# Optimization experiments

Hardware: AMD Instinct MI355X
Metric: run time of the kernel (lower is better)

## Reference

```python
import jax, jax.numpy as jnp
import numpy as np

B = 16          # batch
N = 48          # protein_length
K = 7           # window_size (odd)
PAD = (K - 1) // 2
L = 4 * N - 3   # lattice side from SparseTensor dense_shape
LP = L + 2 * PAD  # zero-padded lattice so every KxKxK window is in-bounds


def setup_inputs() -> dict:
    key = jax.random.key(0)
    k1, k2, k3 = jax.random.split(key, 3)
    acids = jax.random.uniform(k1, (B, N), dtype=jnp.float32)
    mask = jax.random.randint(k2, (B, N), 0, 2).astype(bool)
    # raw integer lattice coords; module maps them via 2*(idx + N-1) into [0, 4N-4]
    idx = jax.random.randint(k3, (B, N, 3), 0, N)
    return {"acids": acids, "mask": mask, "idx": idx}


def _extract_snake(acids, mask, idx2, inter_values, inter_mask, inter_idx):
    # Per-sample: scatter masked acid values + interpolated midpoint values
    # into a dense zero-padded lattice, then gather a KxKxK window around
    # each residue coordinate.  Matches sparse scatter + sparse_slice/to_dense.
    lat = jnp.zeros((LP, LP, LP), dtype=acids.dtype)
    # masked-out rows -> out-of-range index LP, dropped by mode='drop'
    a_idx = jnp.where(mask[:, None], idx2 + PAD, LP)          # [N,3]
    lat = lat.at[a_idx[:, 0], a_idx[:, 1], a_idx[:, 2]].set(acids, mode='drop')
    i_idx = jnp.where(inter_mask[:, None], inter_idx + PAD, LP)  # [N-1,3]
    lat = lat.at[i_idx[:, 0], i_idx[:, 1], i_idx[:, 2]].set(inter_values, mode='drop')

    def window(c):  # c: [3] int, window offset idx2-PAD in unpadded coords == idx2 in padded
        return jax.lax.dynamic_slice(lat, (c[0], c[1], c[2]), (K, K, K))

    regions = jax.vmap(window)(idx2)                          # [N,K,K,K]
    return regions * mask[:, None, None, None].astype(acids.dtype)


def reference(acids, mask, idx):
    idx2 = 2 * (idx + (N - 1))                                # even coords in [0, 4N-4]
    # AVG pool window 2 VALID over sequence dim; midpoints of even coords are exact ints
    inter_idx = (idx2[:, :-1] + idx2[:, 1:]) // 2             # [B,N-1,3]
    # 2 * avg(adjacent acids) + 1 == sum + 1
    inter_values = acids[:, :-1] + acids[:, 1:] + 1.0         # [B,N-1]
    inter_mask = mask[:, 1:]                                  # [B,N-1]
    out = jax.vmap(_extract_snake)(acids, mask, idx2, inter_values, inter_mask, inter_idx)
    return out[..., None]                                     # [B,N,K,K,K,1]
```

## Files before the change

kernel.cpp:

```cpp
#include <hip/hip_runtime.h>

#define BB 16
#define NN 48
#define KK 7
#define PADP 3
#define KCUBE (KK * KK * KK)

__global__ __launch_bounds__(384) void LatticeSnake_kernel(
    const float* __restrict__ acids,
    const int* __restrict__ mask,
    const int* __restrict__ idx,
    float* __restrict__ out)
{
    const int blk = blockIdx.x;
    const int b = blk / NN;
    const int i = blk % NN;
    const int t = threadIdx.x;

    __shared__ int s_idx2[NN][3];
    __shared__ float s_ac[NN];
    __shared__ int s_mk[NN];
    __shared__ int s_ii[NN - 1][3];
    __shared__ float s_iv[NN - 1];

    if (t < NN) {
        s_ac[t] = acids[b * NN + t];
        s_mk[t] = mask[b * NN + t];
#pragma unroll
        for (int d = 0; d < 3; ++d)
            s_idx2[t][d] = 2 * (idx[(b * NN + t) * 3 + d] + (NN - 1));
    }
    __syncthreads();
    if (t < NN - 1) {
#pragma unroll
        for (int d = 0; d < 3; ++d)
            s_ii[t][d] = (s_idx2[t][d] + s_idx2[t + 1][d]) >> 1;
        s_iv[t] = s_ac[t] + s_ac[t + 1] + 1.0f;
    }
    __syncthreads();

    if (t < KCUBE) {
        const int oz = t % KK;
        const int oy = (t / KK) % KK;
        const int ox = t / (KK * KK);
        const int qx = s_idx2[i][0] + ox - PADP;
        const int qy = s_idx2[i][1] + oy - PADP;
        const int qz = s_idx2[i][2] + oz - PADP;

        float v = 0.0f;
        for (int j = 0; j < NN; ++j) {
            if (s_mk[j] && s_idx2[j][0] == qx && s_idx2[j][1] == qy &&
                s_idx2[j][2] == qz)
                v = s_ac[j];
        }
        for (int j = 0; j < NN - 1; ++j) {
            if (s_mk[j + 1] && s_ii[j][0] == qx && s_ii[j][1] == qy &&
                s_ii[j][2] == qz)
                v = s_iv[j];
        }
        if (!s_mk[i]) v = 0.0f;
        out[blk * KCUBE + t] = v;
    }
}

extern "C" void kernel_launch(void* const* d_in, const int* in_sizes, int n_in,
                              void* d_out, int out_size, void* d_ws, size_t ws_size,
                              hipStream_t stream) {
    const float* acids = (const float*)d_in[0];
    const int* mask = (const int*)d_in[1];
    const int* idx = (const int*)d_in[2];
    float* out = (float*)d_out;

    dim3 grid(BB * NN);
    dim3 block(384);
    LatticeSnake_kernel<<<grid, block, 0, stream>>>(acids, mask, idx, out);
}
```

Baseline: 64.50 us.

## Replace per-cell linear search with shared-memory scatter into window

```diff
diff --git a/kernel.cpp b/kernel.cpp
--- a/kernel.cpp
+++ b/kernel.cpp
@@ -22,6 +22,7 @@
     __shared__ int s_mk[NN];
     __shared__ int s_ii[NN - 1][3];
     __shared__ float s_iv[NN - 1];
+    __shared__ int s_win[KCUBE];
 
     if (t < NN) {
         s_ac[t] = acids[b * NN + t];
@@ -30,7 +31,9 @@
         for (int d = 0; d < 3; ++d)
             s_idx2[t][d] = 2 * (idx[(b * NN + t) * 3 + d] + (NN - 1));
     }
+    if (t < KCUBE) s_win[t] = 0;
     __syncthreads();
+
     if (t < NN - 1) {
 #pragma unroll
         for (int d = 0; d < 3; ++d)
@@ -39,26 +42,34 @@
     }
     __syncthreads();
 
+    const int bx = s_idx2[i][0], by = s_idx2[i][1], bz = s_idx2[i][2];
+    if (t < NN) {
+        if (s_mk[t]) {
+            const int ox = s_idx2[t][0] - bx + PADP;
+            const int oy = s_idx2[t][1] - by + PADP;
+            const int oz = s_idx2[t][2] - bz + PADP;
+            if (((unsigned)ox < KK) & ((unsigned)oy < KK) & ((unsigned)oz < KK))
+                atomicMax(&s_win[(ox * KK + oy) * KK + oz], t + 1);
+        }
+    } else if (t < 2 * NN - 1) {
+        const int j = t - NN;
+        if (s_mk[j + 1]) {
+            const int ox = s_ii[j][0] - bx + PADP;
+            const int oy = s_ii[j][1] - by + PADP;
+            const int oz = s_ii[j][2] - bz + PADP;
+            if (((unsigned)ox < KK) & ((unsigned)oy < KK) & ((unsigned)oz < KK))
+                atomicMax(&s_win[(ox * KK + oy) * KK + oz], 64 + j + 1);
+        }
+    }
+    __syncthreads();
+
     if (t < KCUBE) {
-        const int oz = t % KK;
-        const int oy = (t / KK) % KK;
-        const int ox = t / (KK * KK);
-        const int qx = s_idx2[i][0] + ox - PADP;
-        const int qy = s_idx2[i][1] + oy - PADP;
-        const int qz = s_idx2[i][2] + oz - PADP;
-
         float v = 0.0f;
-        for (int j = 0; j < NN; ++j) {
-            if (s_mk[j] && s_idx2[j][0] == qx && s_idx2[j][1] == qy &&
-                s_idx2[j][2] == qz)
-                v = s_ac[j];
+        const int k = s_win[t];
+        if (k > 0 && s_mk[i]) {
+            const int key = k - 1;
+            v = (key >= 64) ? s_iv[key - 64] : s_ac[key];
         }
-        for (int j = 0; j < NN - 1; ++j) {
-            if (s_mk[j + 1] && s_ii[j][0] == qx && s_ii[j][1] == qy &&
-                s_ii[j][2] == qz)
-                v = s_iv[j];
-        }
-        if (!s_mk[i]) v = 0.0f;
         out[blk * KCUBE + t] = v;
     }
 }
```

Result: faster. 57.56 us (-10.8%).
